# Kernel optimization log

Measured on AMD Instinct MI355X. Metric: run time of the kernel, lower is better.

The kernel has to match this reference:

```python
import jax, jax.numpy as jnp
import numpy as np

N, E = 16384, 262144
N_FEAT, N_DIMS, N_CLSS = 128, 64, 40
SIGMA = 1.0
EPS = 1e-8  # torch cosine_similarity / F.normalize eps


def setup_inputs() -> dict:
    key = jax.random.key(0)
    ks = jax.random.split(key, 12)
    d = {
        'x': jax.random.normal(ks[0], (N, N_FEAT), dtype=jnp.float32),
        'edge_index': jax.random.randint(ks[1], (2, E), 0, N, dtype=jnp.int32),
        # SAGEConv1: lin_l (on aggregated neighbors, has bias), lin_r (on root, no bias)
        'W1l': jax.random.normal(ks[2], (N_FEAT, N_DIMS), dtype=jnp.float32) / np.sqrt(N_FEAT),
        'b1': jnp.zeros((N_DIMS,), dtype=jnp.float32),
        'W1r': jax.random.normal(ks[3], (N_FEAT, N_DIMS), dtype=jnp.float32) / np.sqrt(N_FEAT),
        # SAGEConv2
        'W2l': jax.random.normal(ks[4], (N_DIMS, N_DIMS), dtype=jnp.float32) / np.sqrt(N_DIMS),
        'b2': jnp.zeros((N_DIMS,), dtype=jnp.float32),
        'W2r': jax.random.normal(ks[5], (N_DIMS, N_DIMS), dtype=jnp.float32) / np.sqrt(N_DIMS),
        # aux anchor vector
        'aux': jax.random.normal(ks[6], (N_DIMS,), dtype=jnp.float32),
        # classifier Linear(2*n_dims, n_clss)
        'Wc': jax.random.normal(ks[7], (2 * N_DIMS, N_CLSS), dtype=jnp.float32) / np.sqrt(2 * N_DIMS),
        'bc': jnp.zeros((N_CLSS,), dtype=jnp.float32),
    }
    return d


def _sage_conv(x, src, dst, Wl, Wr, b):
    # PyG SAGEConv with mean aggregation: out = lin_l(mean_{j in N(i)} x_j) + lin_r(x_i)
    msg = x[src]  # [E, d]
    agg = jax.ops.segment_sum(msg, dst, num_segments=N)
    cnt = jax.ops.segment_sum(jnp.ones((src.shape[0],), dtype=x.dtype), dst, num_segments=N)
    agg = agg / jnp.maximum(cnt, 1.0)[:, None]  # isolated nodes -> 0
    return agg @ Wl + b + x @ Wr


def _kernel_aggregate(h, aux):
    a = aux / jnp.maximum(jnp.linalg.norm(aux), EPS)           # F.normalize(aux)
    hn = jnp.maximum(jnp.linalg.norm(h, axis=-1), EPS)         # cosine_similarity denom (||a||=1)
    score = (h @ a) / hn                                       # [N]
    diff = score[None, :] - score[:, None]                     # [N, N]
    kappa = jnp.exp(-(diff * diff) / (SIGMA * SIGMA))          # [N, N]
    z = (kappa @ h) / jnp.sum(kappa, axis=1, keepdims=True)
    return z


def reference(x, edge_index, W1l, b1, W1r, W2l, b2, W2r, aux, Wc, bc):
    src, dst = edge_index[0], edge_index[1]
    h = jax.nn.relu(_sage_conv(x, src, dst, W1l, W1r, b1))
    # dropout: eval mode -> identity
    h = _sage_conv(h, src, dst, W2l, W2r, b2)
    z = _kernel_aggregate(h, aux)
    out = jnp.concatenate([h, z], axis=-1) @ Wc + bc
    return out
```

## Files before the change

### kernel.cpp

```cpp
#include <hip/hip_runtime.h>

#define N_NODES 16384
#define N_EDGES 262144
#define F_IN    128
#define DIM     64
#define N_CLS   40
#define KT      16
#define NPART   1024
#define NRED    16
#define MOUT    (KT * (DIM + 1))
#define SLOTS   64
#define EPSF    1e-8f

__device__ __forceinline__ float rlane(float v, int k) {
    return __int_as_float(__builtin_amdgcn_readlane(__float_as_int(v), k));
}
__device__ __forceinline__ int rlane_i(int v, int k) {
    return __builtin_amdgcn_readlane(v, k);
}
__device__ __forceinline__ unsigned short f2bf(float f) {
    unsigned int u = __float_as_uint(f);
    return (unsigned short)((u + 0x7FFFu + ((u >> 16) & 1u)) >> 16);
}
__device__ __forceinline__ float bf2f(unsigned short h) {
    return __uint_as_float(((unsigned int)h) << 16);
}

__global__ __launch_bounds__(256) void k_build(const int* __restrict__ src,
                                               const int* __restrict__ dst,
                                               int* __restrict__ deg,
                                               int* __restrict__ ssrc) {
    int e = blockIdx.x * 256 + threadIdx.x;
    if (e < N_EDGES) {
        const int d = dst[e];
        const int pos = atomicAdd(&deg[d], 1);
        if (pos < SLOTS) ssrc[(d << 6) + pos] = src[e];
    }
}

template<int KDIM>
__global__ __launch_bounds__(256) void k_proj(const float* __restrict__ X,
                                              const float* __restrict__ Wl,
                                              const float* __restrict__ Wr,
                                              unsigned short* __restrict__ p16,
                                              float* __restrict__ r) {
    __shared__ float sWl[KDIM * DIM];
    __shared__ float sWr[KDIM * DIM];
    const int tid = threadIdx.x, lane = tid & 63, w = tid >> 6;
    for (int i = tid; i < KDIM * DIM / 4; i += 256) {
        ((float4*)sWl)[i] = ((const float4*)Wl)[i];
        ((float4*)sWr)[i] = ((const float4*)Wr)[i];
    }
    __syncthreads();

    const int row0 = (blockIdx.x * 4 + w) * 8;
    float xa[8], xb[8];
#pragma unroll
    for (int j = 0; j < 8; ++j) {
        xa[j] = X[(size_t)(row0 + j) * KDIM + lane];
        if constexpr (KDIM == 128) xb[j] = X[(size_t)(row0 + j) * KDIM + 64 + lane];
    }
    float accl[8] = {0.f, 0.f, 0.f, 0.f, 0.f, 0.f, 0.f, 0.f};
    float accr[8] = {0.f, 0.f, 0.f, 0.f, 0.f, 0.f, 0.f, 0.f};
#pragma unroll 8
    for (int k = 0; k < 64; ++k) {
        const float wl = sWl[k * DIM + lane];
        const float wr = sWr[k * DIM + lane];
#pragma unroll
        for (int j = 0; j < 8; ++j) {
            const float xv = rlane(xa[j], k);
            accl[j] = fmaf(xv, wl, accl[j]);
            accr[j] = fmaf(xv, wr, accr[j]);
        }
    }
    if constexpr (KDIM == 128) {
#pragma unroll 8
        for (int k = 0; k < 64; ++k) {
            const float wl = sWl[(64 + k) * DIM + lane];
            const float wr = sWr[(64 + k) * DIM + lane];
#pragma unroll
            for (int j = 0; j < 8; ++j) {
                const float xv = rlane(xb[j], k);
                accl[j] = fmaf(xv, wl, accl[j]);
                accr[j] = fmaf(xv, wr, accr[j]);
            }
        }
    }
#pragma unroll
    for (int j = 0; j < 8; ++j) {
        p16[(size_t)(row0 + j) * DIM + lane] = f2bf(accl[j]);
        r[(size_t)(row0 + j) * DIM + lane]   = accr[j];
    }
}

__device__ __forceinline__ float gather_node(const int* __restrict__ ssrc,
                                             const unsigned short* __restrict__ p16,
                                             int node, int d, int lane) {
    const int eid = (lane < d) ? ssrc[(node << 6) + lane] : 0;
    float acc = 0.f;
    int t = 0;
    for (; t + 8 <= d; t += 8) {
        const int s_0 = rlane_i(eid, t + 0), s_1 = rlane_i(eid, t + 1);
        const int s_2 = rlane_i(eid, t + 2), s_3 = rlane_i(eid, t + 3);
        const int s_4 = rlane_i(eid, t + 4), s_5 = rlane_i(eid, t + 5);
        const int s_6 = rlane_i(eid, t + 6), s_7 = rlane_i(eid, t + 7);
        const unsigned short u0 = p16[(size_t)s_0 * DIM + lane];
        const unsigned short u1 = p16[(size_t)s_1 * DIM + lane];
        const unsigned short u2 = p16[(size_t)s_2 * DIM + lane];
        const unsigned short u3 = p16[(size_t)s_3 * DIM + lane];
        const unsigned short u4 = p16[(size_t)s_4 * DIM + lane];
        const unsigned short u5 = p16[(size_t)s_5 * DIM + lane];
        const unsigned short u6 = p16[(size_t)s_6 * DIM + lane];
        const unsigned short u7 = p16[(size_t)s_7 * DIM + lane];
        acc += ((bf2f(u0) + bf2f(u1)) + (bf2f(u2) + bf2f(u3))) +
               ((bf2f(u4) + bf2f(u5)) + (bf2f(u6) + bf2f(u7)));
    }
    for (; t < d; ++t) {
        const int s = rlane_i(eid, t);
        acc += bf2f(p16[(size_t)s * DIM + lane]);
    }
    return acc;
}

__global__ __launch_bounds__(256) void k_g1p2(const int* __restrict__ ssrc,
                                              const int* __restrict__ deg,
                                              const unsigned short* __restrict__ p1,
                                              const float* __restrict__ r1,
                                              const float* __restrict__ b1,
                                              const float* __restrict__ W2l,
                                              const float* __restrict__ W2r,
                                              unsigned short* __restrict__ p2,
                                              float* __restrict__ r2) {
    __shared__ float sWl[DIM * DIM];
    __shared__ float sWr[DIM * DIM];
    const int tid = threadIdx.x, lane = tid & 63, w = tid >> 6;
    for (int i = tid; i < DIM * DIM / 4; i += 256) {
        ((float4*)sWl)[i] = ((const float4*)W2l)[i];
        ((float4*)sWr)[i] = ((const float4*)W2r)[i];
    }
    __syncthreads();

    const float bb = b1[lane];
    const int node0 = (blockIdx.x * 4 + w) * 4;
    float h1v[4];
#pragma unroll
    for (int jj = 0; jj < 4; ++jj) {
        const int node = node0 + jj;
        const int d = min(deg[node], SLOTS);
        const float acc = gather_node(ssrc, p1, node, d, lane);
        const float val = acc / fmaxf((float)d, 1.f) + bb + r1[(size_t)node * DIM + lane];
        h1v[jj] = fmaxf(val, 0.f);
    }
    float accl[4] = {0.f, 0.f, 0.f, 0.f};
    float accr[4] = {0.f, 0.f, 0.f, 0.f};
#pragma unroll 8
    for (int k = 0; k < DIM; ++k) {
        const float wl = sWl[k * DIM + lane];
        const float wr = sWr[k * DIM + lane];
#pragma unroll
        for (int jj = 0; jj < 4; ++jj) {
            const float hk = rlane(h1v[jj], k);
            accl[jj] = fmaf(hk, wl, accl[jj]);
            accr[jj] = fmaf(hk, wr, accr[jj]);
        }
    }
#pragma unroll
    for (int jj = 0; jj < 4; ++jj) {
        p2[(size_t)(node0 + jj) * DIM + lane] = f2bf(accl[jj]);
        r2[(size_t)(node0 + jj) * DIM + lane] = accr[jj];
    }
}

__global__ __launch_bounds__(256) void k_gather2(const int* __restrict__ ssrc,
                                                 const int* __restrict__ deg,
                                                 const unsigned short* __restrict__ p2,
                                                 const float* __restrict__ r2,
                                                 const float* __restrict__ b2,
                                                 const float* __restrict__ aux,
                                                 float* __restrict__ h2,
                                                 float* __restrict__ score,
                                                 float* __restrict__ Mpart) {
    const int lane = threadIdx.x & 63, w = threadIdx.x >> 6;
    const int tid = threadIdx.x;

    const float bb = b2[lane];
    const float av = aux[lane];
    float an2 = av * av;
#pragma unroll
    for (int off = 32; off >= 1; off >>= 1) an2 += __shfl_xor(an2, off);
    const float anorm = fmaxf(sqrtf(an2), EPSF);

    float accM[KT], accm[KT];
#pragma unroll
    for (int k = 0; k < KT; ++k) { accM[k] = 0.f; accm[k] = 0.f; }

    const int nw = gridDim.x * 4;
    for (int node = blockIdx.x * 4 + w; node < N_NODES; node += nw) {
        const int d = min(deg[node], SLOTS);
        const float acc = gather_node(ssrc, p2, node, d, lane);
        const float hv = acc / fmaxf((float)d, 1.f) + bb + r2[(size_t)node * DIM + lane];
        h2[(size_t)node * DIM + lane] = hv;

        float d1 = hv * av, d2 = hv * hv;
#pragma unroll
        for (int off = 32; off >= 1; off >>= 1) {
            d1 += __shfl_xor(d1, off);
            d2 += __shfl_xor(d2, off);
        }
        const float s = d1 / (anorm * fmaxf(sqrtf(d2), EPSF));
        if (lane == 0) score[node] = s;
        float tt = expf(-s * s);
#pragma unroll
        for (int k = 0; k < KT; ++k) {
            accM[k] = fmaf(tt, hv, accM[k]);
            accm[k] += tt;
            tt *= s;
        }
    }

    __shared__ float sM[KT][DIM];
    __shared__ float smm[KT];
    __syncthreads();
    if (w == 0) {
#pragma unroll
        for (int k = 0; k < KT; ++k) sM[k][lane] = accM[k];
        if (lane == 0)
            for (int k = 0; k < KT; ++k) smm[k] = accm[k];
    }
    __syncthreads();
    if (w != 0) {
        for (int k = 0; k < KT; ++k) atomicAdd(&sM[k][lane], accM[k]);
        if (lane == 0)
            for (int k = 0; k < KT; ++k) atomicAdd(&smm[k], accm[k]);
    }
    __syncthreads();
    float* mp = Mpart + (size_t)blockIdx.x * MOUT;
    const float* sMf = &sM[0][0];
    for (int o = tid; o < KT * DIM; o += 256) mp[o] = sMf[o];
    if (tid < KT) mp[KT * DIM + tid] = smm[tid];
}

__global__ __launch_bounds__(1024) void k_mred(const float* __restrict__ Mpart,
                                               float* __restrict__ Mpart2) {
    const int t = threadIdx.x, B = blockIdx.x;
    float s1 = 0.f, s2 = 0.f;
    for (int b = B * 64; b < B * 64 + 64; ++b) {
        const float* row = Mpart + (size_t)b * MOUT;
        s1 += row[t];
        if (t < MOUT - 1024) s2 += row[1024 + t];
    }
    Mpart2[(size_t)B * MOUT + t] = s1;
    if (t < MOUT - 1024) Mpart2[(size_t)B * MOUT + 1024 + t] = s2;
}

__global__ __launch_bounds__(256) void k_zcls(const float* __restrict__ score,
                                              const float* __restrict__ Mpart2,
                                              const float* __restrict__ h,
                                              const float* __restrict__ Wc,
                                              const float* __restrict__ bc,
                                              float* __restrict__ out) {
    __shared__ float sM[KT * DIM];
    __shared__ float sm[KT];
    __shared__ float sW[2 * DIM * N_CLS];
    __shared__ float sb[N_CLS];
    __shared__ float sh[4][DIM];
    __shared__ float sz[4][DIM];
    const int tid = threadIdx.x;
    for (int idx = tid; idx < KT * DIM; idx += 256) {
        float s = 0.f;
#pragma unroll
        for (int B = 0; B < NRED; ++B) s += Mpart2[(size_t)B * MOUT + idx];
        sM[idx] = s;
    }
    if (tid < KT) {
        float s = 0.f;
#pragma unroll
        for (int B = 0; B < NRED; ++B) s += Mpart2[(size_t)B * MOUT + KT * DIM + tid];
        sm[tid] = s;
    }
    for (int idx = tid; idx < 2 * DIM * N_CLS; idx += 256) sW[idx] = Wc[idx];
    if (tid < N_CLS) sb[tid] = bc[tid];
    __syncthreads();

    const int lane = tid & 63, w = tid >> 6;
    const int gw = blockIdx.x * 4 + w, nw = gridDim.x * 4;
    for (int i = gw; i < N_NODES; i += nw) {
        const float s2 = 2.f * score[i];
        float c = 1.f, num = 0.f, den = 0.f;
#pragma unroll
        for (int k = 0; k < KT; ++k) {
            num = fmaf(c, sM[k * DIM + lane], num);
            den = fmaf(c, sm[k], den);
            c *= s2 * (1.0f / (float)(k + 1));
        }
        sz[w][lane] = num / den;
        sh[w][lane] = h[(size_t)i * DIM + lane];
        if (lane < N_CLS) {
            float acc = sb[lane];
#pragma unroll 8
            for (int k = 0; k < DIM; ++k)
                acc = fmaf(sh[w][k], sW[k * N_CLS + lane], acc);
#pragma unroll 8
            for (int k = 0; k < DIM; ++k)
                acc = fmaf(sz[w][k], sW[(DIM + k) * N_CLS + lane], acc);
            out[(size_t)i * N_CLS + lane] = acc;
        }
    }
}

extern "C" void kernel_launch(void* const* d_in, const int* in_sizes, int n_in,
                              void* d_out, int out_size, void* d_ws, size_t ws_size,
                              hipStream_t stream) {
    const float* x   = (const float*)d_in[0];
    const int*   ei  = (const int*)d_in[1];
    const float* W1l = (const float*)d_in[2];
    const float* b1  = (const float*)d_in[3];
    const float* W1r = (const float*)d_in[4];
    const float* W2l = (const float*)d_in[5];
    const float* b2  = (const float*)d_in[6];
    const float* W2r = (const float*)d_in[7];
    const float* aux = (const float*)d_in[8];
    const float* Wc  = (const float*)d_in[9];
    const float* bc  = (const float*)d_in[10];
    float*       out = (float*)d_out;

    const int* src = ei;
    const int* dst = ei + N_EDGES;

    float*       W  = (float*)d_ws;
    const size_t ND = (size_t)N_NODES * DIM;
    unsigned short* p1 = (unsigned short*)W;
    float* r1    = W + ND / 2;
    unsigned short* p2 = (unsigned short*)(r1 + ND);
    float* r2    = r1 + ND + ND / 2;
    float* h2    = r2 + ND;
    float* score = h2 + ND;
    int*   deg   = (int*)(score + N_NODES);
    float* Mpart = (float*)(deg + N_NODES);
    float* Mpart2= Mpart + (size_t)NPART * MOUT;
    int*   ssrc  = (int*)(Mpart2 + (size_t)NRED * MOUT);

    hipMemsetAsync(deg, 0, N_NODES * sizeof(int), stream);
    k_build<<<N_EDGES / 256, 256, 0, stream>>>(src, dst, deg, ssrc);

    k_proj<F_IN><<<512, 256, 0, stream>>>(x, W1l, W1r, p1, r1);
    k_g1p2<<<N_NODES / 16, 256, 0, stream>>>(ssrc, deg, p1, r1, b1, W2l, W2r, p2, r2);
    k_gather2<<<NPART, 256, 0, stream>>>(ssrc, deg, p2, r2, b2, aux, h2, score, Mpart);
    k_mred<<<NRED, 1024, 0, stream>>>(Mpart, Mpart2);
    k_zcls<<<512, 256, 0, stream>>>(score, Mpart2, h2, Wc, bc, out);
}
```

Measured before the change: 199.8 us.

## Fuse all stages into one cooperative persistent kernel with grid syncs

Replaces the five separate kernel launches (build, projection, gather+proj2, gather2, reduce, classify) with a single cooperative kernel of 512 blocks that separates phases with grid.sync. Each wave keeps its 8 nodes' h2 and score values in registers through to the classifier stage, so the h2 and score round trips to global memory are gone. The final moment reduction now uses atomics into a zeroed buffer. The intent is to cut launch overhead and inter-kernel gaps. In exchange it adds grid-wide barrier costs, fixes occupancy at 2 blocks per CU, and loads W1l and W1r into shared memory one after the other.

```diff
diff --git a/kernel.cpp b/kernel.cpp
--- a/kernel.cpp
+++ b/kernel.cpp
@@ -1,4 +1,7 @@
 #include <hip/hip_runtime.h>
+#include <hip/hip_cooperative_groups.h>
+
+namespace cg = cooperative_groups;
 
 #define N_NODES 16384
 #define N_EDGES 262144
@@ -6,8 +9,8 @@
 #define DIM     64
 #define N_CLS   40
 #define KT      16
-#define NPART   1024
-#define NRED    16
+#define NBLK    512
+#define NPN     8
 #define MOUT    (KT * (DIM + 1))
 #define SLOTS   64
 #define EPSF    1e-8f
@@ -24,73 +27,6 @@
 }
 __device__ __forceinline__ float bf2f(unsigned short h) {
     return __uint_as_float(((unsigned int)h) << 16);
-}
-
-__global__ __launch_bounds__(256) void k_build(const int* __restrict__ src,
-                                               const int* __restrict__ dst,
-                                               int* __restrict__ deg,
-                                               int* __restrict__ ssrc) {
-    int e = blockIdx.x * 256 + threadIdx.x;
-    if (e < N_EDGES) {
-        const int d = dst[e];
-        const int pos = atomicAdd(&deg[d], 1);
-        if (pos < SLOTS) ssrc[(d << 6) + pos] = src[e];
-    }
-}
-
-template<int KDIM>
-__global__ __launch_bounds__(256) void k_proj(const float* __restrict__ X,
-                                              const float* __restrict__ Wl,
-                                              const float* __restrict__ Wr,
-                                              unsigned short* __restrict__ p16,
-                                              float* __restrict__ r) {
-    __shared__ float sWl[KDIM * DIM];
-    __shared__ float sWr[KDIM * DIM];
-    const int tid = threadIdx.x, lane = tid & 63, w = tid >> 6;
-    for (int i = tid; i < KDIM * DIM / 4; i += 256) {
-        ((float4*)sWl)[i] = ((const float4*)Wl)[i];
-        ((float4*)sWr)[i] = ((const float4*)Wr)[i];
-    }
-    __syncthreads();
-
-    const int row0 = (blockIdx.x * 4 + w) * 8;
-    float xa[8], xb[8];
-#pragma unroll
-    for (int j = 0; j < 8; ++j) {
-        xa[j] = X[(size_t)(row0 + j) * KDIM + lane];
-        if constexpr (KDIM == 128) xb[j] = X[(size_t)(row0 + j) * KDIM + 64 + lane];
-    }
-    float accl[8] = {0.f, 0.f, 0.f, 0.f, 0.f, 0.f, 0.f, 0.f};
-    float accr[8] = {0.f, 0.f, 0.f, 0.f, 0.f, 0.f, 0.f, 0.f};
-#pragma unroll 8
-    for (int k = 0; k < 64; ++k) {
-        const float wl = sWl[k * DIM + lane];
-        const float wr = sWr[k * DIM + lane];
-#pragma unroll
-        for (int j = 0; j < 8; ++j) {
-            const float xv = rlane(xa[j], k);
-            accl[j] = fmaf(xv, wl, accl[j]);
-            accr[j] = fmaf(xv, wr, accr[j]);
-        }
-    }
-    if constexpr (KDIM == 128) {
-#pragma unroll 8
-        for (int k = 0; k < 64; ++k) {
-            const float wl = sWl[(64 + k) * DIM + lane];
-            const float wr = sWr[(64 + k) * DIM + lane];
-#pragma unroll
-            for (int j = 0; j < 8; ++j) {
-                const float xv = rlane(xb[j], k);
-                accl[j] = fmaf(xv, wl, accl[j]);
-                accr[j] = fmaf(xv, wr, accr[j]);
-            }
-        }
-    }
-#pragma unroll
-    for (int j = 0; j < 8; ++j) {
-        p16[(size_t)(row0 + j) * DIM + lane] = f2bf(accl[j]);
-        r[(size_t)(row0 + j) * DIM + lane]   = accr[j];
-    }
 }
 
 __device__ __forceinline__ float gather_node(const int* __restrict__ ssrc,
@@ -122,188 +58,232 @@
     return acc;
 }
 
-__global__ __launch_bounds__(256) void k_g1p2(const int* __restrict__ ssrc,
-                                              const int* __restrict__ deg,
-                                              const unsigned short* __restrict__ p1,
-                                              const float* __restrict__ r1,
-                                              const float* __restrict__ b1,
-                                              const float* __restrict__ W2l,
-                                              const float* __restrict__ W2r,
-                                              unsigned short* __restrict__ p2,
-                                              float* __restrict__ r2) {
-    __shared__ float sWl[DIM * DIM];
-    __shared__ float sWr[DIM * DIM];
+__global__ __launch_bounds__(256, 2) void k_mega(
+    const float* __restrict__ x, const int* __restrict__ src, const int* __restrict__ dst,
+    const float* __restrict__ W1l, const float* __restrict__ b1, const float* __restrict__ W1r,
+    const float* __restrict__ W2l, const float* __restrict__ b2, const float* __restrict__ W2r,
+    const float* __restrict__ aux, const float* __restrict__ Wc, const float* __restrict__ bc,
+    float* __restrict__ out,
+    unsigned short* __restrict__ p1, float* __restrict__ r1,
+    unsigned short* __restrict__ p2, float* __restrict__ r2,
+    int* __restrict__ deg, int* __restrict__ ssrc,
+    float* __restrict__ Mpart, float* __restrict__ Mm)
+{
+    cg::grid_group grid = cg::this_grid();
+    __shared__ __align__(16) float smem[8192];
     const int tid = threadIdx.x, lane = tid & 63, w = tid >> 6;
-    for (int i = tid; i < DIM * DIM / 4; i += 256) {
-        ((float4*)sWl)[i] = ((const float4*)W2l)[i];
-        ((float4*)sWr)[i] = ((const float4*)W2r)[i];
-    }
-    __syncthreads();
-
-    const float bb = b1[lane];
-    const int node0 = (blockIdx.x * 4 + w) * 4;
-    float h1v[4];
-#pragma unroll
-    for (int jj = 0; jj < 4; ++jj) {
-        const int node = node0 + jj;
-        const int d = min(deg[node], SLOTS);
-        const float acc = gather_node(ssrc, p1, node, d, lane);
-        const float val = acc / fmaxf((float)d, 1.f) + bb + r1[(size_t)node * DIM + lane];
-        h1v[jj] = fmaxf(val, 0.f);
-    }
-    float accl[4] = {0.f, 0.f, 0.f, 0.f};
-    float accr[4] = {0.f, 0.f, 0.f, 0.f};
-#pragma unroll 8
-    for (int k = 0; k < DIM; ++k) {
-        const float wl = sWl[k * DIM + lane];
-        const float wr = sWr[k * DIM + lane];
-#pragma unroll
-        for (int jj = 0; jj < 4; ++jj) {
-            const float hk = rlane(h1v[jj], k);
-            accl[jj] = fmaf(hk, wl, accl[jj]);
-            accr[jj] = fmaf(hk, wr, accr[jj]);
-        }
-    }
-#pragma unroll
-    for (int jj = 0; jj < 4; ++jj) {
-        p2[(size_t)(node0 + jj) * DIM + lane] = f2bf(accl[jj]);
-        r2[(size_t)(node0 + jj) * DIM + lane] = accr[jj];
-    }
-}
-
-__global__ __launch_bounds__(256) void k_gather2(const int* __restrict__ ssrc,
-                                                 const int* __restrict__ deg,
-                                                 const unsigned short* __restrict__ p2,
-                                                 const float* __restrict__ r2,
-                                                 const float* __restrict__ b2,
-                                                 const float* __restrict__ aux,
-                                                 float* __restrict__ h2,
-                                                 float* __restrict__ score,
-                                                 float* __restrict__ Mpart) {
-    const int lane = threadIdx.x & 63, w = threadIdx.x >> 6;
-    const int tid = threadIdx.x;
-
-    const float bb = b2[lane];
-    const float av = aux[lane];
-    float an2 = av * av;
-#pragma unroll
-    for (int off = 32; off >= 1; off >>= 1) an2 += __shfl_xor(an2, off);
-    const float anorm = fmaxf(sqrtf(an2), EPSF);
-
-    float accM[KT], accm[KT];
-#pragma unroll
-    for (int k = 0; k < KT; ++k) { accM[k] = 0.f; accm[k] = 0.f; }
-
-    const int nw = gridDim.x * 4;
-    for (int node = blockIdx.x * 4 + w; node < N_NODES; node += nw) {
-        const int d = min(deg[node], SLOTS);
-        const float acc = gather_node(ssrc, p2, node, d, lane);
-        const float hv = acc / fmaxf((float)d, 1.f) + bb + r2[(size_t)node * DIM + lane];
-        h2[(size_t)node * DIM + lane] = hv;
-
-        float d1 = hv * av, d2 = hv * hv;
-#pragma unroll
-        for (int off = 32; off >= 1; off >>= 1) {
-            d1 += __shfl_xor(d1, off);
-            d2 += __shfl_xor(d2, off);
-        }
-        const float s = d1 / (anorm * fmaxf(sqrtf(d2), EPSF));
-        if (lane == 0) score[node] = s;
-        float tt = expf(-s * s);
-#pragma unroll
-        for (int k = 0; k < KT; ++k) {
-            accM[k] = fmaf(tt, hv, accM[k]);
-            accm[k] += tt;
-            tt *= s;
-        }
-    }
-
-    __shared__ float sM[KT][DIM];
-    __shared__ float smm[KT];
-    __syncthreads();
-    if (w == 0) {
-#pragma unroll
-        for (int k = 0; k < KT; ++k) sM[k][lane] = accM[k];
-        if (lane == 0)
-            for (int k = 0; k < KT; ++k) smm[k] = accm[k];
-    }
-    __syncthreads();
-    if (w != 0) {
-        for (int k = 0; k < KT; ++k) atomicAdd(&sM[k][lane], accM[k]);
-        if (lane == 0)
-            for (int k = 0; k < KT; ++k) atomicAdd(&smm[k], accm[k]);
-    }
-    __syncthreads();
-    float* mp = Mpart + (size_t)blockIdx.x * MOUT;
-    const float* sMf = &sM[0][0];
-    for (int o = tid; o < KT * DIM; o += 256) mp[o] = sMf[o];
-    if (tid < KT) mp[KT * DIM + tid] = smm[tid];
-}
-
-__global__ __launch_bounds__(1024) void k_mred(const float* __restrict__ Mpart,
-                                               float* __restrict__ Mpart2) {
-    const int t = threadIdx.x, B = blockIdx.x;
-    float s1 = 0.f, s2 = 0.f;
-    for (int b = B * 64; b < B * 64 + 64; ++b) {
-        const float* row = Mpart + (size_t)b * MOUT;
-        s1 += row[t];
-        if (t < MOUT - 1024) s2 += row[1024 + t];
-    }
-    Mpart2[(size_t)B * MOUT + t] = s1;
-    if (t < MOUT - 1024) Mpart2[(size_t)B * MOUT + 1024 + t] = s2;
-}
-
-__global__ __launch_bounds__(256) void k_zcls(const float* __restrict__ score,
-                                              const float* __restrict__ Mpart2,
-                                              const float* __restrict__ h,
-                                              const float* __restrict__ Wc,
-                                              const float* __restrict__ bc,
-                                              float* __restrict__ out) {
-    __shared__ float sM[KT * DIM];
-    __shared__ float sm[KT];
-    __shared__ float sW[2 * DIM * N_CLS];
-    __shared__ float sb[N_CLS];
-    __shared__ float sh[4][DIM];
-    __shared__ float sz[4][DIM];
-    const int tid = threadIdx.x;
-    for (int idx = tid; idx < KT * DIM; idx += 256) {
-        float s = 0.f;
-#pragma unroll
-        for (int B = 0; B < NRED; ++B) s += Mpart2[(size_t)B * MOUT + idx];
-        sM[idx] = s;
-    }
-    if (tid < KT) {
-        float s = 0.f;
-#pragma unroll
-        for (int B = 0; B < NRED; ++B) s += Mpart2[(size_t)B * MOUT + KT * DIM + tid];
-        sm[tid] = s;
-    }
-    for (int idx = tid; idx < 2 * DIM * N_CLS; idx += 256) sW[idx] = Wc[idx];
-    if (tid < N_CLS) sb[tid] = bc[tid];
-    __syncthreads();
-
-    const int lane = tid & 63, w = tid >> 6;
-    const int gw = blockIdx.x * 4 + w, nw = gridDim.x * 4;
-    for (int i = gw; i < N_NODES; i += nw) {
-        const float s2 = 2.f * score[i];
-        float c = 1.f, num = 0.f, den = 0.f;
-#pragma unroll
-        for (int k = 0; k < KT; ++k) {
-            num = fmaf(c, sM[k * DIM + lane], num);
-            den = fmaf(c, sm[k], den);
-            c *= s2 * (1.0f / (float)(k + 1));
-        }
-        sz[w][lane] = num / den;
-        sh[w][lane] = h[(size_t)i * DIM + lane];
-        if (lane < N_CLS) {
-            float acc = sb[lane];
-#pragma unroll 8
-            for (int k = 0; k < DIM; ++k)
-                acc = fmaf(sh[w][k], sW[k * N_CLS + lane], acc);
-#pragma unroll 8
-            for (int k = 0; k < DIM; ++k)
-                acc = fmaf(sz[w][k], sW[(DIM + k) * N_CLS + lane], acc);
-            out[(size_t)i * N_CLS + lane] = acc;
+    const int bid = blockIdx.x;
+    const int wave = bid * 4 + w;
+
+    {
+        for (int e = bid * 256 + tid; e < N_EDGES; e += NBLK * 256) {
+            const int d = dst[e];
+            const int pos = atomicAdd(&deg[d], 1);
+            if (pos < SLOTS) ssrc[(d << 6) + pos] = src[e];
+        }
+    }
+    {
+        for (int i = tid; i < F_IN * DIM / 4; i += 256)
+            ((float4*)smem)[i] = ((const float4*)W1l)[i];
+        const int row0 = wave * NPN;
+        float xa[NPN], xb[NPN];
+#pragma unroll
+        for (int j = 0; j < NPN; ++j) {
+            xa[j] = x[(size_t)(row0 + j) * F_IN + lane];
+            xb[j] = x[(size_t)(row0 + j) * F_IN + 64 + lane];
+        }
+        __syncthreads();
+        {
+            float acc[NPN];
+#pragma unroll
+            for (int j = 0; j < NPN; ++j) acc[j] = 0.f;
+#pragma unroll 8
+            for (int k = 0; k < 64; ++k) {
+                const float wl = smem[k * DIM + lane];
+#pragma unroll
+                for (int j = 0; j < NPN; ++j) acc[j] = fmaf(rlane(xa[j], k), wl, acc[j]);
+            }
+#pragma unroll 8
+            for (int k = 0; k < 64; ++k) {
+                const float wl = smem[(64 + k) * DIM + lane];
+#pragma unroll
+                for (int j = 0; j < NPN; ++j) acc[j] = fmaf(rlane(xb[j], k), wl, acc[j]);
+            }
+#pragma unroll
+            for (int j = 0; j < NPN; ++j) p1[(size_t)(row0 + j) * DIM + lane] = f2bf(acc[j]);
+        }
+        __syncthreads();
+        for (int i = tid; i < F_IN * DIM / 4; i += 256)
+            ((float4*)smem)[i] = ((const float4*)W1r)[i];
+        __syncthreads();
+        {
+            float acc[NPN];
+#pragma unroll
+            for (int j = 0; j < NPN; ++j) acc[j] = 0.f;
+#pragma unroll 8
+            for (int k = 0; k < 64; ++k) {
+                const float wl = smem[k * DIM + lane];
+#pragma unroll
+                for (int j = 0; j < NPN; ++j) acc[j] = fmaf(rlane(xa[j], k), wl, acc[j]);
+            }
+#pragma unroll 8
+            for (int k = 0; k < 64; ++k) {
+                const float wl = smem[(64 + k) * DIM + lane];
+#pragma unroll
+                for (int j = 0; j < NPN; ++j) acc[j] = fmaf(rlane(xb[j], k), wl, acc[j]);
+            }
+#pragma unroll
+            for (int j = 0; j < NPN; ++j) r1[(size_t)(row0 + j) * DIM + lane] = acc[j];
+        }
+    }
+    grid.sync();
+
+    {
+        for (int i = tid; i < DIM * DIM / 4; i += 256) {
+            ((float4*)smem)[i]          = ((const float4*)W2l)[i];
+            ((float4*)(smem + 4096))[i] = ((const float4*)W2r)[i];
+        }
+        const float bb = b1[lane];
+        const int node0 = wave * NPN;
+        float h1v[NPN];
+#pragma unroll
+        for (int jj = 0; jj < NPN; ++jj) {
+            const int node = node0 + jj;
+            const int d = min(deg[node], SLOTS);
+            const float acc = gather_node(ssrc, p1, node, d, lane);
+            const float val = acc / fmaxf((float)d, 1.f) + bb + r1[(size_t)node * DIM + lane];
+            h1v[jj] = fmaxf(val, 0.f);
+        }
+        __syncthreads();
+        float accl[NPN], accr[NPN];
+#pragma unroll
+        for (int j = 0; j < NPN; ++j) { accl[j] = 0.f; accr[j] = 0.f; }
+#pragma unroll 8
+        for (int k = 0; k < DIM; ++k) {
+            const float wl = smem[k * DIM + lane];
+            const float wr = smem[4096 + k * DIM + lane];
+#pragma unroll
+            for (int jj = 0; jj < NPN; ++jj) {
+                const float hk = rlane(h1v[jj], k);
+                accl[jj] = fmaf(hk, wl, accl[jj]);
+                accr[jj] = fmaf(hk, wr, accr[jj]);
+            }
+        }
+#pragma unroll
+        for (int jj = 0; jj < NPN; ++jj) {
+            p2[(size_t)(node0 + jj) * DIM + lane] = f2bf(accl[jj]);
+            r2[(size_t)(node0 + jj) * DIM + lane] = accr[jj];
+        }
+    }
+    grid.sync();
+
+    float hv2[NPN], sc[NPN];
+    {
+        const float bb = b2[lane];
+        const float av = aux[lane];
+        float an2 = av * av;
+#pragma unroll
+        for (int off = 32; off >= 1; off >>= 1) an2 += __shfl_xor(an2, off);
+        const float anorm = fmaxf(sqrtf(an2), EPSF);
+
+        float accM[KT], accm[KT];
+#pragma unroll
+        for (int k = 0; k < KT; ++k) { accM[k] = 0.f; accm[k] = 0.f; }
+
+        const int node0 = wave * NPN;
+#pragma unroll
+        for (int jj = 0; jj < NPN; ++jj) {
+            const int node = node0 + jj;
+            const int d = min(deg[node], SLOTS);
+            const float acc = gather_node(ssrc, p2, node, d, lane);
+            const float hv = acc / fmaxf((float)d, 1.f) + bb + r2[(size_t)node * DIM + lane];
+            hv2[jj] = hv;
+            float d1 = hv * av, d2 = hv * hv;
+#pragma unroll
+            for (int off = 32; off >= 1; off >>= 1) {
+                d1 += __shfl_xor(d1, off);
+                d2 += __shfl_xor(d2, off);
+            }
+            const float s = d1 / (anorm * fmaxf(sqrtf(d2), EPSF));
+            sc[jj] = s;
+            float tt = expf(-s * s);
+#pragma unroll
+            for (int k = 0; k < KT; ++k) {
+                accM[k] = fmaf(tt, hv, accM[k]);
+                accm[k] += tt;
+                tt *= s;
+            }
+        }
+
+        float* sM  = smem;
+        float* smm = smem + KT * DIM;
+        __syncthreads();
+        if (w == 0) {
+#pragma unroll
+            for (int k = 0; k < KT; ++k) sM[k * DIM + lane] = accM[k];
+            if (lane == 0)
+                for (int k = 0; k < KT; ++k) smm[k] = accm[k];
+        }
+        __syncthreads();
+        if (w != 0) {
+            for (int k = 0; k < KT; ++k) atomicAdd(&sM[k * DIM + lane], accM[k]);
+            if (lane == 0)
+                for (int k = 0; k < KT; ++k) atomicAdd(&smm[k], accm[k]);
+        }
+        __syncthreads();
+        float* mp = Mpart + (size_t)bid * MOUT;
+        for (int o = tid; o < KT * DIM; o += 256) mp[o] = sM[o];
+        if (tid < KT) mp[KT * DIM + tid] = smm[tid];
+    }
+    grid.sync();
+
+    if (bid < 16) {
+        for (int o = tid; o < MOUT; o += 256) {
+            float s = 0.f;
+            for (int b = bid * 32; b < bid * 32 + 32; ++b)
+                s += Mpart[(size_t)b * MOUT + o];
+            atomicAdd(&Mm[o], s);
+        }
+    }
+    grid.sync();
+
+    {
+        float* sWc = smem;
+        float* sbc = smem + 5120;
+        float* sMo = smem + 5160;
+        float* smv = smem + 6184;
+        float* sh  = smem + 6200;
+        float* sz  = smem + 6456;
+        for (int i = tid; i < 2 * DIM * N_CLS; i += 256) sWc[i] = Wc[i];
+        if (tid < N_CLS) sbc[tid] = bc[tid];
+        for (int i = tid; i < KT * DIM; i += 256) sMo[i] = Mm[i];
+        if (tid < KT) smv[tid] = Mm[KT * DIM + tid];
+        __syncthreads();
+
+        const int node0 = wave * NPN;
+#pragma unroll
+        for (int jj = 0; jj < NPN; ++jj) {
+            const int node = node0 + jj;
+            const float s2 = 2.f * sc[jj];
+            float c = 1.f, num = 0.f, den = 0.f;
+#pragma unroll
+            for (int k = 0; k < KT; ++k) {
+                num = fmaf(c, sMo[k * DIM + lane], num);
+                den = fmaf(c, smv[k], den);
+                c *= s2 * (1.0f / (float)(k + 1));
+            }
+            sz[w * DIM + lane] = num / den;
+            sh[w * DIM + lane] = hv2[jj];
+            if (lane < N_CLS) {
+                float a = sbc[lane];
+#pragma unroll 8
+                for (int k = 0; k < DIM; ++k)
+                    a = fmaf(sh[w * DIM + k], sWc[k * N_CLS + lane], a);
+#pragma unroll 8
+                for (int k = 0; k < DIM; ++k)
+                    a = fmaf(sz[w * DIM + k], sWc[(DIM + k) * N_CLS + lane], a);
+                out[(size_t)node * N_CLS + lane] = a;
+            }
         }
     }
 }
@@ -333,19 +313,21 @@
     float* r1    = W + ND / 2;
     unsigned short* p2 = (unsigned short*)(r1 + ND);
     float* r2    = r1 + ND + ND / 2;
-    float* h2    = r2 + ND;
-    float* score = h2 + ND;
-    int*   deg   = (int*)(score + N_NODES);
-    float* Mpart = (float*)(deg + N_NODES);
-    float* Mpart2= Mpart + (size_t)NPART * MOUT;
-    int*   ssrc  = (int*)(Mpart2 + (size_t)NRED * MOUT);
-
-    hipMemsetAsync(deg, 0, N_NODES * sizeof(int), stream);
-    k_build<<<N_EDGES / 256, 256, 0, stream>>>(src, dst, deg, ssrc);
-
-    k_proj<F_IN><<<512, 256, 0, stream>>>(x, W1l, W1r, p1, r1);
-    k_g1p2<<<N_NODES / 16, 256, 0, stream>>>(ssrc, deg, p1, r1, b1, W2l, W2r, p2, r2);
-    k_gather2<<<NPART, 256, 0, stream>>>(ssrc, deg, p2, r2, b2, aux, h2, score, Mpart);
-    k_mred<<<NRED, 1024, 0, stream>>>(Mpart, Mpart2);
-    k_zcls<<<512, 256, 0, stream>>>(score, Mpart2, h2, Wc, bc, out);
-}
+    int*   deg   = (int*)(r2 + ND);
+    float* Mm    = (float*)(deg + N_NODES);
+    float* Mpart = Mm + MOUT;
+    int*   ssrc  = (int*)(Mpart + (size_t)NBLK * MOUT);
+
+    hipMemsetAsync(deg, 0, (N_NODES + MOUT) * sizeof(float), stream);
+
+    void* args[] = {
+        (void*)&x, (void*)&src, (void*)&dst,
+        (void*)&W1l, (void*)&b1, (void*)&W1r,
+        (void*)&W2l, (void*)&b2, (void*)&W2r,
+        (void*)&aux, (void*)&Wc, (void*)&bc,
+        (void*)&out,
+        (void*)&p1, (void*)&r1, (void*)&p2, (void*)&r2,
+        (void*)&deg, (void*)&ssrc, (void*)&Mpart, (void*)&Mm,
+    };
+    hipLaunchCooperativeKernel((void*)k_mega, dim3(NBLK), dim3(256), args, 0, stream);
+}
```

After: 441.3 us. 121% more time.

## Fuse edge-bucket build into layer-1 projection and widen gather grids

Applied to the files above, without the earlier changes.

Merges the edge-bucketing kernel into the first projection kernel so one launch does both the atomic slot fill and the X·W products, removing a kernel launch and its serialization. The layer-1 gather kernel now handles 2 nodes per wave instead of 4 with twice the blocks, and the layer-2 gather kernel uses 4096 blocks with one node per wave instead of a grid-stride loop. This raises parallelism for the latency-bound gathers, at the cost of four times as many partial-moment rows written and then reduced by the reduction kernel.

```diff
diff --git a/kernel.cpp b/kernel.cpp
--- a/kernel.cpp
+++ b/kernel.cpp
@@ -6,7 +6,7 @@
 #define DIM     64
 #define N_CLS   40
 #define KT      16
-#define NPART   1024
+#define NPART   4096
 #define NRED    16
 #define MOUT    (KT * (DIM + 1))
 #define SLOTS   64
@@ -24,73 +24,6 @@
 }
 __device__ __forceinline__ float bf2f(unsigned short h) {
     return __uint_as_float(((unsigned int)h) << 16);
-}
-
-__global__ __launch_bounds__(256) void k_build(const int* __restrict__ src,
-                                               const int* __restrict__ dst,
-                                               int* __restrict__ deg,
-                                               int* __restrict__ ssrc) {
-    int e = blockIdx.x * 256 + threadIdx.x;
-    if (e < N_EDGES) {
-        const int d = dst[e];
-        const int pos = atomicAdd(&deg[d], 1);
-        if (pos < SLOTS) ssrc[(d << 6) + pos] = src[e];
-    }
-}
-
-template<int KDIM>
-__global__ __launch_bounds__(256) void k_proj(const float* __restrict__ X,
-                                              const float* __restrict__ Wl,
-                                              const float* __restrict__ Wr,
-                                              unsigned short* __restrict__ p16,
-                                              float* __restrict__ r) {
-    __shared__ float sWl[KDIM * DIM];
-    __shared__ float sWr[KDIM * DIM];
-    const int tid = threadIdx.x, lane = tid & 63, w = tid >> 6;
-    for (int i = tid; i < KDIM * DIM / 4; i += 256) {
-        ((float4*)sWl)[i] = ((const float4*)Wl)[i];
-        ((float4*)sWr)[i] = ((const float4*)Wr)[i];
-    }
-    __syncthreads();
-
-    const int row0 = (blockIdx.x * 4 + w) * 8;
-    float xa[8], xb[8];
-#pragma unroll
-    for (int j = 0; j < 8; ++j) {
-        xa[j] = X[(size_t)(row0 + j) * KDIM + lane];
-        if constexpr (KDIM == 128) xb[j] = X[(size_t)(row0 + j) * KDIM + 64 + lane];
-    }
-    float accl[8] = {0.f, 0.f, 0.f, 0.f, 0.f, 0.f, 0.f, 0.f};
-    float accr[8] = {0.f, 0.f, 0.f, 0.f, 0.f, 0.f, 0.f, 0.f};
-#pragma unroll 8
-    for (int k = 0; k < 64; ++k) {
-        const float wl = sWl[k * DIM + lane];
-        const float wr = sWr[k * DIM + lane];
-#pragma unroll
-        for (int j = 0; j < 8; ++j) {
-            const float xv = rlane(xa[j], k);
-            accl[j] = fmaf(xv, wl, accl[j]);
-            accr[j] = fmaf(xv, wr, accr[j]);
-        }
-    }
-    if constexpr (KDIM == 128) {
-#pragma unroll 8
-        for (int k = 0; k < 64; ++k) {
-            const float wl = sWl[(64 + k) * DIM + lane];
-            const float wr = sWr[(64 + k) * DIM + lane];
-#pragma unroll
-            for (int j = 0; j < 8; ++j) {
-                const float xv = rlane(xb[j], k);
-                accl[j] = fmaf(xv, wl, accl[j]);
-                accr[j] = fmaf(xv, wr, accr[j]);
-            }
-        }
-    }
-#pragma unroll
-    for (int j = 0; j < 8; ++j) {
-        p16[(size_t)(row0 + j) * DIM + lane] = f2bf(accl[j]);
-        r[(size_t)(row0 + j) * DIM + lane]   = accr[j];
-    }
 }
 
 __device__ __forceinline__ float gather_node(const int* __restrict__ ssrc,
@@ -122,6 +55,69 @@
     return acc;
 }
 
+__global__ __launch_bounds__(256) void k_projb(const float* __restrict__ X,
+                                               const float* __restrict__ Wl,
+                                               const float* __restrict__ Wr,
+                                               const int* __restrict__ src,
+                                               const int* __restrict__ dst,
+                                               int* __restrict__ deg,
+                                               int* __restrict__ ssrc,
+                                               unsigned short* __restrict__ p16,
+                                               float* __restrict__ r) {
+    const int tid = threadIdx.x, lane = tid & 63, w = tid >> 6;
+
+    for (int e = blockIdx.x * 256 + tid; e < N_EDGES; e += 512 * 256) {
+        const int d = dst[e];
+        const int pos = atomicAdd(&deg[d], 1);
+        if (pos < SLOTS) ssrc[(d << 6) + pos] = src[e];
+    }
+
+    __shared__ float sWl[F_IN * DIM];
+    __shared__ float sWr[F_IN * DIM];
+    for (int i = tid; i < F_IN * DIM / 4; i += 256) {
+        ((float4*)sWl)[i] = ((const float4*)Wl)[i];
+        ((float4*)sWr)[i] = ((const float4*)Wr)[i];
+    }
+    __syncthreads();
+
+    const int row0 = (blockIdx.x * 4 + w) * 8;
+    float xa[8], xb[8];
+#pragma unroll
+    for (int j = 0; j < 8; ++j) {
+        xa[j] = X[(size_t)(row0 + j) * F_IN + lane];
+        xb[j] = X[(size_t)(row0 + j) * F_IN + 64 + lane];
+    }
+    float accl[8] = {0.f, 0.f, 0.f, 0.f, 0.f, 0.f, 0.f, 0.f};
+    float accr[8] = {0.f, 0.f, 0.f, 0.f, 0.f, 0.f, 0.f, 0.f};
+#pragma unroll 8
+    for (int k = 0; k < 64; ++k) {
+        const float wl = sWl[k * DIM + lane];
+        const float wr = sWr[k * DIM + lane];
+#pragma unroll
+        for (int j = 0; j < 8; ++j) {
+            const float xv = rlane(xa[j], k);
+            accl[j] = fmaf(xv, wl, accl[j]);
+            accr[j] = fmaf(xv, wr, accr[j]);
+        }
+    }
+#pragma unroll 8
+    for (int k = 0; k < 64; ++k) {
+        const float wl = sWl[(64 + k) * DIM + lane];
+        const float wr = sWr[(64 + k) * DIM + lane];
+#pragma unroll
+        for (int j = 0; j < 8; ++j) {
+            const float xv = rlane(xb[j], k);
+            accl[j] = fmaf(xv, wl, accl[j]);
+            accr[j] = fmaf(xv, wr, accr[j]);
+        }
+    }
+#pragma unroll
+    for (int j = 0; j < 8; ++j) {
+        p16[(size_t)(row0 + j) * DIM + lane] = f2bf(accl[j]);
+        r[(size_t)(row0 + j) * DIM + lane]   = accr[j];
+    }
+}
+
 __global__ __launch_bounds__(256) void k_g1p2(const int* __restrict__ ssrc,
                                               const int* __restrict__ deg,
                                               const unsigned short* __restrict__ p1,
@@ -141,31 +137,31 @@
     __syncthreads();
 
     const float bb = b1[lane];
-    const int node0 = (blockIdx.x * 4 + w) * 4;
-    float h1v[4];
-#pragma unroll
-    for (int jj = 0; jj < 4; ++jj) {
+    const int node0 = (blockIdx.x * 4 + w) * 2;
+    float h1v[2];
+#pragma unroll
+    for (int jj = 0; jj < 2; ++jj) {
         const int node = node0 + jj;
         const int d = min(deg[node], SLOTS);
         const float acc = gather_node(ssrc, p1, node, d, lane);
         const float val = acc / fmaxf((float)d, 1.f) + bb + r1[(size_t)node * DIM + lane];
         h1v[jj] = fmaxf(val, 0.f);
     }
-    float accl[4] = {0.f, 0.f, 0.f, 0.f};
-    float accr[4] = {0.f, 0.f, 0.f, 0.f};
+    float accl[2] = {0.f, 0.f};
+    float accr[2] = {0.f, 0.f};
 #pragma unroll 8
     for (int k = 0; k < DIM; ++k) {
         const float wl = sWl[k * DIM + lane];
         const float wr = sWr[k * DIM + lane];
 #pragma unroll
-        for (int jj = 0; jj < 4; ++jj) {
+        for (int jj = 0; jj < 2; ++jj) {
             const float hk = rlane(h1v[jj], k);
             accl[jj] = fmaf(hk, wl, accl[jj]);
             accr[jj] = fmaf(hk, wr, accr[jj]);
         }
     }
 #pragma unroll
-    for (int jj = 0; jj < 4; ++jj) {
+    for (int jj = 0; jj < 2; ++jj) {
         p2[(size_t)(node0 + jj) * DIM + lane] = f2bf(accl[jj]);
         r2[(size_t)(node0 + jj) * DIM + lane] = accr[jj];
     }
@@ -194,8 +190,8 @@
 #pragma unroll
     for (int k = 0; k < KT; ++k) { accM[k] = 0.f; accm[k] = 0.f; }
 
-    const int nw = gridDim.x * 4;
-    for (int node = blockIdx.x * 4 + w; node < N_NODES; node += nw) {
+    {
+        const int node = blockIdx.x * 4 + w;
         const int d = min(deg[node], SLOTS);
         const float acc = gather_node(ssrc, p2, node, d, lane);
         const float hv = acc / fmaxf((float)d, 1.f) + bb + r2[(size_t)node * DIM + lane];
@@ -244,7 +240,7 @@
                                                float* __restrict__ Mpart2) {
     const int t = threadIdx.x, B = blockIdx.x;
     float s1 = 0.f, s2 = 0.f;
-    for (int b = B * 64; b < B * 64 + 64; ++b) {
+    for (int b = B * 256; b < B * 256 + 256; ++b) {
         const float* row = Mpart + (size_t)b * MOUT;
         s1 += row[t];
         if (t < MOUT - 1024) s2 += row[1024 + t];
@@ -341,10 +337,8 @@
     int*   ssrc  = (int*)(Mpart2 + (size_t)NRED * MOUT);
 
     hipMemsetAsync(deg, 0, N_NODES * sizeof(int), stream);
-    k_build<<<N_EDGES / 256, 256, 0, stream>>>(src, dst, deg, ssrc);
-
-    k_proj<F_IN><<<512, 256, 0, stream>>>(x, W1l, W1r, p1, r1);
-    k_g1p2<<<N_NODES / 16, 256, 0, stream>>>(ssrc, deg, p1, r1, b1, W2l, W2r, p2, r2);
+    k_projb<<<512, 256, 0, stream>>>(x, W1l, W1r, src, dst, deg, ssrc, p1, r1);
+    k_g1p2<<<N_NODES / 8, 256, 0, stream>>>(ssrc, deg, p1, r1, b1, W2l, W2r, p2, r2);
     k_gather2<<<NPART, 256, 0, stream>>>(ssrc, deg, p2, r2, b2, aux, h2, score, Mpart);
     k_mred<<<NRED, 1024, 0, stream>>>(Mpart, Mpart2);
     k_zcls<<<512, 256, 0, stream>>>(score, Mpart2, h2, Wc, bc, out);
```

Result: slower. 297.0 us (+48.6%).
